# Kernel tuning notes

Measured on AMD Instinct MI355X. Metric: run time of the kernel, lower is better.

The kernel has to match this reference:

```python
import jax, jax.numpy as jnp
import numpy as np

N = 384      # max_nodes
H = 256      # layers[0] == layers[1] == layers[2]
Z = 128      # dim_z
ED = 128     # edge_dim
AH = ED // 2 # attention hidden

# complete directed graph: combinations (i<j) then reversed pairs
_i, _j = np.triu_indices(N, k=1)
_SRC = jnp.asarray(np.concatenate([_i, _j]), dtype=jnp.int32)  # edge_index[0]
_DST = jnp.asarray(np.concatenate([_j, _i]), dtype=jnp.int32)  # edge_index[1]


def setup_inputs() -> dict:
    key = jax.random.key(0)
    ks = jax.random.split(key, 16)
    def p(k, shape, fan_in):
        return jax.random.normal(k, shape, dtype=jnp.float32) * (1.0 / np.sqrt(fan_in))
    return {
        "z": jax.random.normal(ks[0], (1, Z), dtype=jnp.float32),
        # GRU (torch layout: W_ih [3H, Z], W_hh [3H, H]; gate order r, z, n)
        "gru_Wih": p(ks[1], (3 * H, Z), Z),
        "gru_Whh": p(ks[2], (3 * H, H), H),
        "gru_bih": jnp.zeros((3 * H,), jnp.float32),
        "gru_bhh": jnp.zeros((3 * H,), jnp.float32),
        # edge_generator MLP: 2H -> 4H -> ED
        "eg_W1": p(ks[3], (2 * H, 4 * H), 2 * H), "eg_b1": jnp.zeros((4 * H,), jnp.float32),
        "eg_W2": p(ks[4], (4 * H, ED), 4 * H),   "eg_b2": jnp.zeros((ED,), jnp.float32),
        # attention MLPs: (ED+H) -> ED//2 -> 1
        "att0_W1": p(ks[5], (ED + H, AH), ED + H), "att0_b1": jnp.zeros((AH,), jnp.float32),
        "att0_W2": p(ks[6], (AH, 1), AH),           "att0_b2": jnp.zeros((1,), jnp.float32),
        "att1_W1": p(ks[7], (ED + H, AH), ED + H), "att1_b1": jnp.zeros((AH,), jnp.float32),
        "att1_W2": p(ks[8], (AH, 1), AH),           "att1_b2": jnp.zeros((1,), jnp.float32),
        # EdgeConv output linears: H -> H
        "conv0_W": p(ks[9], (H, H), H),  "conv0_b": jnp.zeros((H,), jnp.float32),
        "conv1_W": p(ks[10], (H, H), H), "conv1_b": jnp.zeros((H,), jnp.float32),
    }


def _forward(z, gru_Wih, gru_Whh, gru_bih, gru_bhh,
             eg_W1, eg_b1, eg_W2, eg_b2,
             att0_W1, att0_b1, att0_W2, att0_b2,
             att1_W1, att1_b1, att1_W2, att1_b2,
             conv0_W, conv0_b, conv1_W, conv1_b):
    # --- GRU node generation: input is the same latent z at every step ---
    gi = z[0] @ gru_Wih.T + gru_bih            # [3H], constant per step
    gir, giz, gin = jnp.split(gi, 3)
    def step(h, _):
        gh = h @ gru_Whh.T + gru_bhh
        ghr, ghz, ghn = jnp.split(gh, 3)
        r = jax.nn.sigmoid(gir + ghr)
        u = jax.nn.sigmoid(giz + ghz)
        n = jnp.tanh(gin + r * ghn)
        h2 = (1.0 - u) * n + u * h
        return h2, h2
    _, nodes = jax.lax.scan(step, jnp.zeros((H,), z.dtype), None, length=N)  # [N, H]

    # --- edge features over the complete directed graph ---
    pairs = jnp.concatenate([nodes[_SRC], nodes[_DST]], axis=-1)            # [E, 2H]
    edges = jax.nn.relu(pairs @ eg_W1 + eg_b1) @ eg_W2 + eg_b2              # [E, ED]

    # --- EdgeConv: gather src, attention MLP gate, scatter-sum, linear ---
    def conv(x, aW1, ab1, aW2, ab2, W, b):
        xs = x[_SRC]                                                        # [E, H]
        a_in = jnp.concatenate([edges, xs], axis=-1)                        # [E, ED+H]
        att = jax.nn.sigmoid(jax.nn.relu(a_in @ aW1 + ab1) @ aW2 + ab2)     # [E, 1]
        agg = jax.ops.segment_sum(att * xs, _DST, num_segments=N)           # [N, H]
        return agg @ W + b

    x = jax.nn.relu(conv(nodes, att0_W1, att0_b1, att0_W2, att0_b2, conv0_W, conv0_b))
    x = conv(x, att1_W1, att1_b1, att1_W2, att1_b2, conv1_W, conv1_b)
    return jnp.sum(x, axis=0)                                               # [H]


def reference(z, gru_Wih, gru_Whh, gru_bih, gru_bhh,
              eg_W1, eg_b1, eg_W2, eg_b2,
              att0_W1, att0_b1, att0_W2, att0_b2,
              att1_W1, att1_b1, att1_W2, att1_b2,
              conv0_W, conv0_b, conv1_W, conv1_b):
    return _forward(z, gru_Wih, gru_Whh, gru_bih, gru_bhh,
                    eg_W1, eg_b1, eg_W2, eg_b2,
                    att0_W1, att0_b1, att0_W2, att0_b2,
                    att1_W1, att1_b1, att1_W2, att1_b2,
                    conv0_W, conv0_b, conv1_W, conv1_b)
```

## Files before the change

kernel.cpp:

```cpp
#include <hip/hip_runtime.h>
#include <hip/hip_fp16.h>
#include <cstdint>

#define DEV static __device__ __forceinline__

typedef _Float16 h2v __attribute__((ext_vector_type(2)));
typedef _Float16 half8 __attribute__((ext_vector_type(8)));
typedef float float4v __attribute__((ext_vector_type(4)));

union U32H2 { uint32_t u; _Float16 f[2]; };

DEV uint32_t pack_f2(float a, float b) {
    auto p = __builtin_amdgcn_cvt_pkrtz(a, b);
    return __builtin_bit_cast(uint32_t, p);
}

DEV half8 bc8(uint4 v) { return __builtin_bit_cast(half8, v); }

DEV float sigmoidf_(float x) { return 1.0f / (1.0f + __expf(-x)); }
DEV float tanh_fast(float x) { float e = __expf(-2.0f*x); return (1.0f - e) / (1.0f + e); }

DEV void gl_lds16(const void* gsrc, void* ldst) {
    __builtin_amdgcn_global_load_lds(
        (const __attribute__((address_space(1))) uint32_t*)gsrc,
        (__attribute__((address_space(3))) uint32_t*)ldst, 16, 0, 0);
}

static const size_t OFF_W16T  = 0;
static const size_t OFF_GI    = 98304;
static const size_t OFF_CC    = 99072;
static const size_t OFF_BF    = 99200;
static const size_t OFF_NODES = 164736;
static const size_t OFF_PF    = 263040;
static const size_t OFF_QF    = 459648;
static const size_t OFF_R0    = 656256;
static const size_t OFF_R1    = 680832;
static const size_t OFF_TT    = 705408;
static const size_t OFF_ATT0  = 10142592;
static const size_t OFF_ATT1  = 10290048;
static const size_t OFF_AGG   = 10437504;
static const size_t OFF_X0    = 10535808;
static const size_t OFF_CS    = 10634112;
static const size_t OFF_V     = 10634496;
static const size_t WS_TOTAL  = 10634752;

__global__ void k_prep_w16(const float* __restrict__ Whh, uint32_t* __restrict__ WL) {
    int o4 = blockIdx.x * 256 + threadIdx.x;
    int c = o4 >> 9, t = o4 & 511;
    int rt = c >> 3, kt = c & 7;
    int lane = t & 63, wv = t >> 6;
    int m = (wv*6 + rt)*16 + (lane & 15);
    int k0 = kt*32 + (lane >> 4)*8;
    const float* src = Whh + m*256 + k0;
    uint4 o;
    o.x = pack_f2(src[0], src[1]);
    o.y = pack_f2(src[2], src[3]);
    o.z = pack_f2(src[4], src[5]);
    o.w = pack_f2(src[6], src[7]);
    ((uint4*)WL)[o4] = o;
}

__global__ void k_prep_gi(const float* __restrict__ z, const float* __restrict__ Wih,
                          const float* __restrict__ bih, float* __restrict__ gi) {
    int o = blockIdx.x * 256 + threadIdx.x;
    float acc = bih[o];
    for (int i = 0; i < 128; ++i) acc += Wih[o*128 + i] * z[i];
    gi[o] = acc;
}

__global__ void k_prep_cc(const float* __restrict__ eg_b2, const float* __restrict__ a0W1,
                          const float* __restrict__ a1W1, float* __restrict__ cc) {
    int t = threadIdx.x;
    const float* A = (t < 64) ? a0W1 : a1W1;
    int j = t & 63;
    float acc = 0.f;
    for (int i = 0; i < 128; ++i) acc += eg_b2[i] * A[i*64 + j];
    cc[t] = acc;
}

__global__ void k_prep_w2a(const float* __restrict__ eg_W2, const float* __restrict__ a0W1,
                           const float* __restrict__ a1W1, uint32_t* __restrict__ BF) {
    int idx = blockIdx.x * 256 + threadIdx.x;
    int k2 = idx >> 7, n = idx & 127;
    const float* A = (n < 64) ? (a0W1 + n) : (a1W1 + (n - 64));
    const float* w0 = eg_W2 + (2*k2) * 128;
    float a = 0.f, b = 0.f;
    for (int i = 0; i < 128; ++i) {
        float av = A[i*64];
        a += w0[i] * av;
        b += w0[128 + i] * av;
    }
    int kk = k2 >> 4, jgrp = (k2 >> 2) & 3, sub = k2 & 3;
    int lane = jgrp*16 + (n & 15), t = n >> 4;
    BF[((kk*8 + t)*64 + lane)*4 + sub] = pack_f2(a, b);
}

__global__ void __launch_bounds__(512, 2)
k_gru(const float* __restrict__ gi, const float* __restrict__ bhh,
      const uint32_t* __restrict__ WL, float* __restrict__ nodes) {
    int tid = threadIdx.x;
    int lane = tid & 63, wv = tid >> 6;
    __shared__ __align__(16) _Float16 hh16[256];
    __shared__ float ghs[768];

    uint4 w[48];
    const uint4* wl4 = (const uint4*)WL;
    #pragma unroll
    for (int c = 0; c < 48; ++c) w[c] = wl4[c*512 + tid];
    #pragma unroll
    for (int c = 0; c < 48; ++c)
        asm volatile("" : "+a"(w[c].x), "+a"(w[c].y), "+a"(w[c].z), "+a"(w[c].w));

    float gir = 0.f, giz = 0.f, gin = 0.f, bh0 = 0.f, bh1 = 0.f, bh2 = 0.f;
    if (tid < 256) {
        gir = gi[tid]; giz = gi[256 + tid]; gin = gi[512 + tid];
        bh0 = bhh[tid]; bh1 = bhh[256 + tid]; bh2 = bhh[512 + tid];
    }
    float h = 0.f;
    if (tid < 128) ((uint32_t*)hh16)[tid] = 0u;
    __syncthreads();

    int kq = lane >> 4;
    bool writer = (lane & 15) == 0;
    int rowbase = wv*6*16 + kq*4;

    for (int t = 0; t < 384; ++t) {
        float4v d[6];
        #pragma unroll
        for (int rt = 0; rt < 6; ++rt) d[rt] = 0.f;

        half8 bcur = bc8(*(const uint4*)(hh16 + 0*32 + kq*8));
        #pragma unroll
        for (int kt = 0; kt < 8; ++kt) {
            half8 bnext;
            if (kt < 7) bnext = bc8(*(const uint4*)(hh16 + (kt+1)*32 + kq*8));
            #pragma unroll
            for (int rt = 0; rt < 6; ++rt)
                d[rt] = __builtin_amdgcn_mfma_f32_16x16x32_f16(
                    bc8(w[rt*8 + kt]), bcur, d[rt], 0, 0, 0);
            bcur = bnext;
        }

        if (writer) {
            #pragma unroll
            for (int rt = 0; rt < 6; ++rt)
                *(float4v*)(ghs + rowbase + rt*16) = d[rt];
        }
        __syncthreads();
        if (tid < 256) {
            float a0 = ghs[tid]       + bh0;
            float a1 = ghs[256 + tid] + bh1;
            float a2 = ghs[512 + tid] + bh2;
            float rg = sigmoidf_(gir + a0);
            float u  = sigmoidf_(giz + a1);
            float n  = tanh_fast(gin + rg * a2);
            h = (1.f - u) * n + u * h;
            hh16[tid] = (_Float16)h;
            nodes[t*256 + tid] = h;
        }
        __syncthreads();
    }
}

__global__ void k_pq(const float* __restrict__ nodes, const float* __restrict__ eg_W1,
                     const float* __restrict__ eg_b1, const float* __restrict__ a0W1,
                     const float* __restrict__ a0b1, const float* __restrict__ cc,
                     uint32_t* __restrict__ PF, uint32_t* __restrict__ QF,
                     float* __restrict__ R0) {
    int tid = threadIdx.x;
    int s0 = blockIdx.x * 4;
    __shared__ float ns[4][256];
    #pragma unroll
    for (int q = 0; q < 4; ++q) ns[q][tid] = nodes[(s0+q)*256 + tid];
    __syncthreads();

    int k0 = tid * 4;
    float acc[4][4];
    #pragma unroll
    for (int q = 0; q < 4; ++q) { acc[q][0]=0;acc[q][1]=0;acc[q][2]=0;acc[q][3]=0; }
    for (int i = 0; i < 256; ++i) {
        float4 wv = *(const float4*)&eg_W1[i*1024 + k0];
        #pragma unroll
        for (int q = 0; q < 4; ++q) {
            float nv = ns[q][i];
            acc[q][0] += nv*wv.x; acc[q][1] += nv*wv.y;
            acc[q][2] += nv*wv.z; acc[q][3] += nv*wv.w;
        }
    }
    float4 bv = *(const float4*)&eg_b1[k0];
    {
        int kk = k0 >> 5;
        int lgrp = ((k0 >> 3) & 3) * 16;
        int sub = (k0 & 7) >> 1;
        #pragma unroll
        for (int q = 0; q < 4; ++q) {
            int s = s0 + q, g = s >> 4, srow = s & 15;
            uint2 pw;
            pw.x = pack_f2(acc[q][0] + bv.x, acc[q][1] + bv.y);
            pw.y = pack_f2(acc[q][2] + bv.z, acc[q][3] + bv.w);
            *(uint2*)(PF + (((g*32 + kk)*64 + lgrp + srow) << 2) + sub) = pw;
        }
    }

    #pragma unroll
    for (int q = 0; q < 4; ++q) { acc[q][0]=0;acc[q][1]=0;acc[q][2]=0;acc[q][3]=0; }
    for (int i = 0; i < 256; ++i) {
        float4 wv = *(const float4*)&eg_W1[(256+i)*1024 + k0];
        #pragma unroll
        for (int q = 0; q < 4; ++q) {
            float nv = ns[q][i];
            acc[q][0] += nv*wv.x; acc[q][1] += nv*wv.y;
            acc[q][2] += nv*wv.z; acc[q][3] += nv*wv.w;
        }
    }
    #pragma unroll
    for (int q = 0; q < 4; ++q) {
        uint2 pw;
        pw.x = pack_f2(acc[q][0], acc[q][1]);
        pw.y = pack_f2(acc[q][2], acc[q][3]);
        ((uint2*)QF)[(s0+q)*256 + tid] = pw;
    }

    int srow = tid >> 6, j = tid & 63;
    float racc = a0b1[j] + cc[j];
    for (int i = 0; i < 256; ++i) racc += ns[srow][i] * a0W1[(128+i)*64 + j];
    R0[(s0+srow)*64 + j] = racc;
}

__global__ void __launch_bounds__(256, 2)
k_phaseA_mfma(const uint32_t* __restrict__ PF, const uint32_t* __restrict__ QF,
              const uint32_t* __restrict__ BF, uint32_t* __restrict__ TT) {
    __shared__ __align__(16) char smem[69632];
    uint4* Qs4 = (uint4*)smem;
    uint4* Ps4 = (uint4*)(smem + 32768);
    uint4* Bs4 = (uint4*)(smem + 36864);

    int tid = threadIdx.x;
    int lane = tid & 63, wv = tid >> 6;
    int g = blockIdx.x, d0 = blockIdx.y * 16;

    {
        const char* src = (const char*)(QF + (size_t)d0 * 512);
        for (int off = wv*1024 + lane*16; off < 32768; off += 4096)
            gl_lds16(src + off, (char*)Qs4 + off);
    }

    float4v acc[4][8];
    #pragma unroll
    for (int t = 0; t < 4; ++t)
        #pragma unroll
        for (int n = 0; n < 8; ++n) acc[t][n] = 0.f;

    for (int c = 0; c < 8; ++c) {
        __syncthreads();
        {
            const char* psrc = (const char*)(PF + (size_t)(g*32 + c*4) * 256);
            for (int off = wv*1024 + lane*16; off < 4096; off += 4096)
                gl_lds16(psrc + off, (char*)Ps4 + off);
            const char* bsrc = (const char*)(BF + (size_t)c * 8192);
            for (int off = wv*1024 + lane*16; off < 32768; off += 4096)
                gl_lds16(bsrc + off, (char*)Bs4 + off);
        }
        __syncthreads();

        #pragma unroll
        for (int kkl = 0; kkl < 4; ++kkl) {
            int kkg = c*4 + kkl;
            half8 b[8];
            #pragma unroll
            for (int n = 0; n < 8; ++n) b[n] = bc8(Bs4[(kkl*8 + n)*64 + lane]);
            half8 p8 = bc8(Ps4[kkl*64 + lane]);
            #pragma unroll
            for (int t = 0; t < 4; ++t) {
                half8 q8 = bc8(Qs4[(wv*4 + t)*128 + kkg*4 + (lane >> 4)]);
                half8 x = p8 + q8;
                half8 z = 0;
                x = __builtin_elementwise_max(x, z);
                #pragma unroll
                for (int n = 0; n < 8; ++n)
                    acc[t][n] = __builtin_amdgcn_mfma_f32_16x16x32_f16(x, b[n], acc[t][n], 0, 0, 0);
            }
        }
    }

    _Float16* epi = (_Float16*)(smem + 36864);
    int cn = lane & 15, rhi = (lane >> 4) * 4;
    for (int half = 0; half < 2; ++half) {
        __syncthreads();
        #pragma unroll
        for (int t = 0; t < 4; ++t) {
            int dl = wv*4 + t;
            #pragma unroll
            for (int n = 0; n < 4; ++n) {
                int j = n*16 + cn;
                float4v v = acc[t][half*4 + n];
                #pragma unroll
                for (int r = 0; r < 4; ++r)
                    epi[((rhi + r)*16 + dl)*64 + j] = (_Float16)v[r];
            }
        }
        __syncthreads();
        int srow = tid >> 4, dl = tid & 15;
        const uint4* src = (const uint4*)(epi + tid*64);
        uint4* dst = (uint4*)(TT + ((size_t)((g*16 + srow)*384 + d0 + dl))*64 + half*32);
        #pragma unroll
        for (int q = 0; q < 8; ++q) dst[q] = src[q];
    }
}

__global__ void k_att(const uint32_t* __restrict__ TT, const float* __restrict__ R,
                      const float* __restrict__ w2, const float* __restrict__ b2,
                      int off, float* __restrict__ ATT) {
    int p = blockIdx.x * 256 + threadIdx.x;
    int s = p / 384, d = p - s * 384;
    __shared__ float w2s[64];
    if (threadIdx.x < 64) w2s[threadIdx.x] = w2[threadIdx.x];
    __syncthreads();
    const uint4* tp = (const uint4*)(TT + (size_t)p*64 + off);
    const float* rp = R + s*64;
    float logit = b2[0];
    #pragma unroll
    for (int m = 0; m < 8; ++m) {
        uint4 tv = tp[m];
        uint32_t us[4] = {tv.x, tv.y, tv.z, tv.w};
        #pragma unroll
        for (int q = 0; q < 4; ++q) {
            U32H2 c; c.u = us[q];
            int j = m*8 + q*2;
            float h0 = fmaxf((float)c.f[0] + rp[j],   0.f);
            float h1 = fmaxf((float)c.f[1] + rp[j+1], 0.f);
            logit += h0*w2s[j] + h1*w2s[j+1];
        }
    }
    float a = 1.f / (1.f + __expf(-logit));
    ATT[p] = (s == d) ? 0.f : a;
}

__global__ void __launch_bounds__(256)
k_agg(const float* __restrict__ ATT, const float* __restrict__ X,
      float* __restrict__ AGG) {
    int tid = threadIdx.x;
    int d0 = blockIdx.x * 16;
    __shared__ float att_s[16][17];
    float acc[16];
    #pragma unroll
    for (int dl = 0; dl < 16; ++dl) acc[dl] = 0.f;

    for (int s0 = 0; s0 < 384; s0 += 16) {
        __syncthreads();
        {
            int row = tid >> 4, col = tid & 15;
            att_s[row][col] = ATT[(s0 + row)*384 + d0 + col];
        }
        __syncthreads();
        #pragma unroll 4
        for (int ss = 0; ss < 16; ++ss) {
            float x = X[(s0 + ss)*256 + tid];
            #pragma unroll
            for (int dl = 0; dl < 16; ++dl) acc[dl] += att_s[ss][dl] * x;
        }
    }
    #pragma unroll
    for (int dl = 0; dl < 16; ++dl)
        AGG[(d0 + dl)*256 + tid] = acc[dl];
}

__global__ void k_x0r1(const float* __restrict__ AGG, const float* __restrict__ W,
                       const float* __restrict__ b, const float* __restrict__ a1W1,
                       const float* __restrict__ a1b1, const float* __restrict__ cc,
                       float* __restrict__ X0, float* __restrict__ R1) {
    int d = blockIdx.x, tid = threadIdx.x;
    __shared__ float ag[256];
    __shared__ float xs[256];
    ag[tid] = AGG[d*256 + tid];
    __syncthreads();
    float acc = b[tid];
    for (int i = 0; i < 256; ++i) acc += ag[i] * W[i*256 + tid];
    acc = fmaxf(acc, 0.f);
    X0[d*256 + tid] = acc;
    xs[tid] = acc;
    __syncthreads();
    if (tid < 64) {
        float r = a1b1[tid] + cc[64 + tid];
        for (int i = 0; i < 256; ++i) r += xs[i] * a1W1[(128+i)*64 + tid];
        R1[d*64 + tid] = r;
    }
}

__global__ void k_colsum(const float* __restrict__ ATT, float* __restrict__ CS) {
    int s = blockIdx.x, t = threadIdx.x;
    float acc = 0.f;
    for (int d = t; d < 384; d += 64) acc += ATT[s*384 + d];
    for (int o = 32; o > 0; o >>= 1) acc += __shfl_down(acc, o, 64);
    if (t == 0) CS[s] = acc;
}

__global__ void k_v(const float* __restrict__ CS, const float* __restrict__ X0,
                    float* __restrict__ V) {
    int tid = threadIdx.x;
    __shared__ float cs[384];
    for (int q = tid; q < 384; q += 256) cs[q] = CS[q];
    __syncthreads();
    float acc = 0.f;
    for (int s = 0; s < 384; s += 4) {
        acc += cs[s]*X0[s*256 + tid] + cs[s+1]*X0[(s+1)*256 + tid]
             + cs[s+2]*X0[(s+2)*256 + tid] + cs[s+3]*X0[(s+3)*256 + tid];
    }
    V[tid] = acc;
}

__global__ void k_out(const float* __restrict__ V, const float* __restrict__ W,
                      const float* __restrict__ b, float* __restrict__ out) {
    int tid = threadIdx.x;
    __shared__ float vs[256];
    vs[tid] = V[tid];
    __syncthreads();
    float acc = 384.f * b[tid];
    for (int i = 0; i < 256; ++i) acc += vs[i] * W[i*256 + tid];
    out[tid] = acc;
}

extern "C" void kernel_launch(void* const* d_in, const int* in_sizes, int n_in,
                              void* d_out, int out_size, void* d_ws, size_t ws_size,
                              hipStream_t stream) {
    if (ws_size < WS_TOTAL * sizeof(uint32_t)) return;

    const float* z    = (const float*)d_in[0];
    const float* Wih  = (const float*)d_in[1];
    const float* Whh  = (const float*)d_in[2];
    const float* bih  = (const float*)d_in[3];
    const float* bhh  = (const float*)d_in[4];
    const float* egW1 = (const float*)d_in[5];
    const float* egb1 = (const float*)d_in[6];
    const float* egW2 = (const float*)d_in[7];
    const float* egb2 = (const float*)d_in[8];
    const float* a0W1 = (const float*)d_in[9];
    const float* a0b1 = (const float*)d_in[10];
    const float* a0W2 = (const float*)d_in[11];
    const float* a0b2 = (const float*)d_in[12];
    const float* a1W1 = (const float*)d_in[13];
    const float* a1b1 = (const float*)d_in[14];
    const float* a1W2 = (const float*)d_in[15];
    const float* a1b2 = (const float*)d_in[16];
    const float* c0W  = (const float*)d_in[17];
    const float* c0b  = (const float*)d_in[18];
    const float* c1W  = (const float*)d_in[19];
    const float* c1b  = (const float*)d_in[20];

    uint32_t* ws   = (uint32_t*)d_ws;
    uint32_t* WL   = ws + OFF_W16T;
    float*    gi   = (float*)(ws + OFF_GI);
    float*    cc   = (float*)(ws + OFF_CC);
    uint32_t* BF   = ws + OFF_BF;
    float*    nodes= (float*)(ws + OFF_NODES);
    uint32_t* PF   = ws + OFF_PF;
    uint32_t* QF   = ws + OFF_QF;
    float*    R0   = (float*)(ws + OFF_R0);
    float*    R1   = (float*)(ws + OFF_R1);
    uint32_t* TT   = ws + OFF_TT;
    float*    ATT0 = (float*)(ws + OFF_ATT0);
    float*    ATT1 = (float*)(ws + OFF_ATT1);
    float*    AGG  = (float*)(ws + OFF_AGG);
    float*    X0   = (float*)(ws + OFF_X0);
    float*    CS   = (float*)(ws + OFF_CS);
    float*    V    = (float*)(ws + OFF_V);
    float*    out  = (float*)d_out;

    hipLaunchKernelGGL(k_prep_w16,    dim3(96),  dim3(256), 0, stream, Whh, WL);
    hipLaunchKernelGGL(k_prep_gi,     dim3(3),   dim3(256), 0, stream, z, Wih, bih, gi);
    hipLaunchKernelGGL(k_prep_cc,     dim3(1),   dim3(128), 0, stream, egb2, a0W1, a1W1, cc);
    hipLaunchKernelGGL(k_prep_w2a,    dim3(256), dim3(256), 0, stream, egW2, a0W1, a1W1, BF);
    hipLaunchKernelGGL(k_gru,         dim3(1),   dim3(512), 0, stream, gi, bhh, WL, nodes);
    hipLaunchKernelGGL(k_pq,          dim3(96),  dim3(256), 0, stream, nodes, egW1, egb1, a0W1, a0b1, cc, PF, QF, R0);
    hipLaunchKernelGGL(k_phaseA_mfma, dim3(24, 24), dim3(256), 0, stream, PF, QF, BF, TT);
    hipLaunchKernelGGL(k_att,         dim3(576), dim3(256), 0, stream, TT, R0, a0W2, a0b2, 0,  ATT0);
    hipLaunchKernelGGL(k_agg,         dim3(24),  dim3(256), 0, stream, ATT0, nodes, AGG);
    hipLaunchKernelGGL(k_x0r1,        dim3(384), dim3(256), 0, stream, AGG, c0W, c0b, a1W1, a1b1, cc, X0, R1);
    hipLaunchKernelGGL(k_att,         dim3(576), dim3(256), 0, stream, TT, R1, a1W2, a1b2, 32, ATT1);
    hipLaunchKernelGGL(k_colsum,      dim3(384), dim3(64),  0, stream, ATT1, CS);
    hipLaunchKernelGGL(k_v,           dim3(1),   dim3(256), 0, stream, CS, X0, V);
    hipLaunchKernelGGL(k_out,         dim3(1),   dim3(256), 0, stream, V, c1W, c1b, out);
}
```

Baseline: 797.6 us.

## Compute GRU gates in MFMA lanes with double-buffered hidden state, one barrier

Permutes the W_hh fragment layout so each wave's MFMA outputs hold matching r, z and n rows for 32 hidden units. The gate math then runs directly from the accumulator registers instead of going through an LDS staging buffer. The hidden state is double-buffered in LDS, so each sequential step needs one barrier instead of two, and the r/z biases are folded into the precomputed input term. The intent is to shorten the serial 384-step GRU critical path. The cost is redundant gate math across lanes and hand-written exp2/rcp approximations.

```diff
diff --git a/kernel.cpp b/kernel.cpp
--- a/kernel.cpp
+++ b/kernel.cpp
@@ -18,12 +18,21 @@
 DEV half8 bc8(uint4 v) { return __builtin_bit_cast(half8, v); }
 
 DEV float sigmoidf_(float x) { return 1.0f / (1.0f + __expf(-x)); }
-DEV float tanh_fast(float x) { float e = __expf(-2.0f*x); return (1.0f - e) / (1.0f + e); }
 
 DEV void gl_lds16(const void* gsrc, void* ldst) {
     __builtin_amdgcn_global_load_lds(
         (const __attribute__((address_space(1))) uint32_t*)gsrc,
         (__attribute__((address_space(3))) uint32_t*)ldst, 16, 0, 0);
+}
+
+DEV float pick4(float4v lo, float4v hi, int bsel, int r) {
+    float v0 = bsel ? hi[0] : lo[0];
+    float v1 = bsel ? hi[1] : lo[1];
+    float v2 = bsel ? hi[2] : lo[2];
+    float v3 = bsel ? hi[3] : lo[3];
+    float x01 = (r & 1) ? v1 : v0;
+    float x23 = (r & 1) ? v3 : v2;
+    return (r & 2) ? x23 : x01;
 }
 
 static const size_t OFF_W16T  = 0;
@@ -49,9 +58,9 @@
     int c = o4 >> 9, t = o4 & 511;
     int rt = c >> 3, kt = c & 7;
     int lane = t & 63, wv = t >> 6;
-    int m = (wv*6 + rt)*16 + (lane & 15);
+    int row = (rt >> 1) * 256 + wv * 32 + ((rt & 1) << 4) + (lane & 15);
     int k0 = kt*32 + (lane >> 4)*8;
-    const float* src = Whh + m*256 + k0;
+    const float* src = Whh + row*256 + k0;
     uint4 o;
     o.x = pack_f2(src[0], src[1]);
     o.y = pack_f2(src[2], src[3]);
@@ -61,11 +70,13 @@
 }
 
 __global__ void k_prep_gi(const float* __restrict__ z, const float* __restrict__ Wih,
-                          const float* __restrict__ bih, float* __restrict__ gi) {
+                          const float* __restrict__ bih, const float* __restrict__ bhh,
+                          float* __restrict__ gs) {
     int o = blockIdx.x * 256 + threadIdx.x;
     float acc = bih[o];
+    if (o < 512) acc += bhh[o];
     for (int i = 0; i < 128; ++i) acc += Wih[o*128 + i] * z[i];
-    gi[o] = acc;
+    gs[o] = acc;
 }
 
 __global__ void k_prep_cc(const float* __restrict__ eg_b2, const float* __restrict__ a0W1,
@@ -96,69 +107,77 @@
 }
 
 __global__ void __launch_bounds__(512, 2)
-k_gru(const float* __restrict__ gi, const float* __restrict__ bhh,
+k_gru(const float* __restrict__ gs, const float* __restrict__ bhh,
       const uint32_t* __restrict__ WL, float* __restrict__ nodes) {
     int tid = threadIdx.x;
     int lane = tid & 63, wv = tid >> 6;
-    __shared__ __align__(16) _Float16 hh16[256];
-    __shared__ float ghs[768];
+    int kq = lane >> 4, c = lane & 15;
+    __shared__ __align__(16) _Float16 hh16[512];
 
     uint4 w[48];
     const uint4* wl4 = (const uint4*)WL;
     #pragma unroll
-    for (int c = 0; c < 48; ++c) w[c] = wl4[c*512 + tid];
-    #pragma unroll
-    for (int c = 0; c < 48; ++c)
-        asm volatile("" : "+a"(w[c].x), "+a"(w[c].y), "+a"(w[c].z), "+a"(w[c].w));
-
-    float gir = 0.f, giz = 0.f, gin = 0.f, bh0 = 0.f, bh1 = 0.f, bh2 = 0.f;
-    if (tid < 256) {
-        gir = gi[tid]; giz = gi[256 + tid]; gin = gi[512 + tid];
-        bh0 = bhh[tid]; bh1 = bhh[256 + tid]; bh2 = bhh[512 + tid];
-    }
+    for (int cc = 0; cc < 48; ++cc) w[cc] = wl4[cc*512 + tid];
+    #pragma unroll
+    for (int cc = 0; cc < 48; ++cc)
+        asm volatile("" : "+a"(w[cc].x), "+a"(w[cc].y), "+a"(w[cc].z), "+a"(w[cc].w));
+
+    const float L2E = 1.44269504088896f;
+    int r = c & 3, bsel = (c >> 2) & 1;
+    int i_loc = kq*4 + r + bsel*16;
+    int gidx = wv*32 + i_loc;
+    float pr = -L2E * gs[gidx];
+    float pz = -L2E * gs[256 + gidx];
+    float gin_l = gs[512 + gidx];
+    float bn_l  = bhh[512 + gidx];
+    float pn = -2.f * L2E * gin_l;
+    bool active = (c < 8);
+
     float h = 0.f;
-    if (tid < 128) ((uint32_t*)hh16)[tid] = 0u;
-    __syncthreads();
-
-    int kq = lane >> 4;
-    bool writer = (lane & 15) == 0;
-    int rowbase = wv*6*16 + kq*4;
-
+    if (tid < 256) ((uint32_t*)hh16)[tid] = 0u;
+    __syncthreads();
+
+    const float4v z4 = {0.f, 0.f, 0.f, 0.f};
+    int par = 0;
     for (int t = 0; t < 384; ++t) {
+        const _Float16* hb = hh16 + par*256 + kq*8;
+        uint4 b[8];
+        #pragma unroll
+        for (int kt = 0; kt < 8; ++kt) b[kt] = *(const uint4*)(hb + kt*32);
+
         float4v d[6];
         #pragma unroll
-        for (int rt = 0; rt < 6; ++rt) d[rt] = 0.f;
-
-        half8 bcur = bc8(*(const uint4*)(hh16 + 0*32 + kq*8));
-        #pragma unroll
-        for (int kt = 0; kt < 8; ++kt) {
-            half8 bnext;
-            if (kt < 7) bnext = bc8(*(const uint4*)(hh16 + (kt+1)*32 + kq*8));
+        for (int rt = 0; rt < 6; ++rt)
+            d[rt] = __builtin_amdgcn_mfma_f32_16x16x32_f16(bc8(w[rt*8]), bc8(b[0]), z4, 0, 0, 0);
+        #pragma unroll
+        for (int kt = 1; kt < 8; ++kt)
             #pragma unroll
             for (int rt = 0; rt < 6; ++rt)
-                d[rt] = __builtin_amdgcn_mfma_f32_16x16x32_f16(
-                    bc8(w[rt*8 + kt]), bcur, d[rt], 0, 0, 0);
-            bcur = bnext;
-        }
-
-        if (writer) {
-            #pragma unroll
-            for (int rt = 0; rt < 6; ++rt)
-                *(float4v*)(ghs + rowbase + rt*16) = d[rt];
-        }
-        __syncthreads();
-        if (tid < 256) {
-            float a0 = ghs[tid]       + bh0;
-            float a1 = ghs[256 + tid] + bh1;
-            float a2 = ghs[512 + tid] + bh2;
-            float rg = sigmoidf_(gir + a0);
-            float u  = sigmoidf_(giz + a1);
-            float n  = tanh_fast(gin + rg * a2);
-            h = (1.f - u) * n + u * h;
-            hh16[tid] = (_Float16)h;
-            nodes[t*256 + tid] = h;
-        }
-        __syncthreads();
+                d[rt] = __builtin_amdgcn_mfma_f32_16x16x32_f16(bc8(w[rt*8 + kt]), bc8(b[kt]), d[rt], 0, 0, 0);
+
+        float ghr = pick4(d[0], d[1], bsel, r);
+        float ghz = pick4(d[2], d[3], bsel, r);
+        float ghn = pick4(d[4], d[5], bsel, r);
+
+        float er = __builtin_amdgcn_exp2f(__builtin_fmaf(ghr, -L2E, pr));
+        float rg = __builtin_amdgcn_rcpf(1.f + er);
+        float eu = __builtin_amdgcn_exp2f(__builtin_fmaf(ghz, -L2E, pz));
+        float u  = __builtin_amdgcn_rcpf(1.f + eu);
+        float tm = ghn + bn_l;
+        float q  = __builtin_fmaf(rg * tm, -2.f * L2E, pn);
+        float e2 = __builtin_amdgcn_exp2f(q);
+        float nn = __builtin_fmaf(2.f, __builtin_amdgcn_rcpf(1.f + e2), -1.f);
+        h = nn + u * (h - nn);
+
+        if (active) {
+            hh16[(par ^ 1)*256 + gidx] = (_Float16)h;
+            nodes[t*256 + gidx] = h;
+        }
+        asm volatile("s_waitcnt lgkmcnt(0)" ::: "memory");
+        __builtin_amdgcn_sched_barrier(0);
+        __builtin_amdgcn_s_barrier();
+        __builtin_amdgcn_sched_barrier(0);
+        par ^= 1;
     }
 }
 
@@ -467,7 +486,7 @@
     float*    out  = (float*)d_out;
 
     hipLaunchKernelGGL(k_prep_w16,    dim3(96),  dim3(256), 0, stream, Whh, WL);
-    hipLaunchKernelGGL(k_prep_gi,     dim3(3),   dim3(256), 0, stream, z, Wih, bih, gi);
+    hipLaunchKernelGGL(k_prep_gi,     dim3(3),   dim3(256), 0, stream, z, Wih, bih, bhh, gi);
     hipLaunchKernelGGL(k_prep_cc,     dim3(1),   dim3(128), 0, stream, egb2, a0W1, a1W1, cc);
     hipLaunchKernelGGL(k_prep_w2a,    dim3(256), dim3(256), 0, stream, egW2, a0W1, a1W1, BF);
     hipLaunchKernelGGL(k_gru,         dim3(1),   dim3(512), 0, stream, gi, bhh, WL, nodes);
```

Result: faster. 704.8 us (-11.6%).
